# Kernel tuning notes

Measured on AMD Instinct MI355X. Metric: run time of the kernel, lower is better.

Reference implementation:

```python
import jax, jax.numpy as jnp
import numpy as np

HEAD_DIM = 64
N_HEADS = 16
DIM = 1024
EPS = 1e-6
GRID = 32  # make_axial_pos(32, 32)


def _make_theta(head_dim=HEAD_DIM, n_heads=N_HEADS):
    hd8 = head_dim // 8
    nh2 = n_heads // 2
    freqs = np.exp(np.linspace(np.log(np.pi), np.log(10 * np.pi), hd8 * nh2 + 1)[:-1])
    freqs = freqs.reshape(hd8, nh2).T  # (nh2, hd8)
    # axial positions on a 32x32 grid, cell centers in [-1, 1]
    p = np.linspace(-1.0, 1.0, GRID + 1)
    p = (p[:-1] + p[1:]) / 2
    pos = np.stack(np.meshgrid(p, p, indexing='ij'), axis=-1).reshape(GRID * GRID, 2)
    pos = np.concatenate([np.zeros((1, 2)), pos], axis=0)  # (1025, 2)
    th1 = np.concatenate([pos[:-1, None, 0:1] * freqs, pos[:-1, None, 1:2] * freqs], axis=-1)
    th2 = np.concatenate([pos[1:, None, 0:1] * freqs, pos[1:, None, 1:2] * freqs], axis=-1)
    # (seq=1024, n_heads, head_dim//4)
    return np.concatenate([th1, th2], axis=1).astype(np.float32)


def setup_inputs() -> dict:
    key = jax.random.key(0)
    k1, k2, k3 = jax.random.split(key, 3)
    B, S = 8, 1024
    x = jax.random.normal(k1, (B, S, DIM), dtype=jnp.float32)
    scale = jnp.ones((DIM,), dtype=jnp.float32)
    w_qkv = jax.random.normal(k2, (3 * DIM, DIM), dtype=jnp.float32) * 0.02
    w_out = jax.random.normal(k3, (DIM, DIM), dtype=jnp.float32) * 0.02
    theta = jnp.asarray(_make_theta())
    return {"x": x, "scale": scale, "w_qkv": w_qkv, "w_out": w_out, "theta": theta}


def _rms_norm(x, scale, eps):
    xf = x.astype(jnp.float32)
    mean_sq = jnp.mean(xf * xf, axis=-1, keepdims=True)
    s = scale.astype(jnp.float32) * jax.lax.rsqrt(mean_sq + eps)
    return x * s.astype(x.dtype)


def _rope(x, theta):
    # x: (B, H, S, D); theta: (H, S, d) with d = D // 4 -> rotates first D//2 dims
    d = theta.shape[-1]
    cos = jnp.cos(theta)
    sin = jnp.sin(theta)
    x1, x2, rest = x[..., :d], x[..., d:2 * d], x[..., 2 * d:]
    y1 = x1 * cos - x2 * sin
    y2 = x2 * cos + x1 * sin
    return jnp.concatenate([y1, y2, rest], axis=-1)


def reference(x, scale, w_qkv, w_out, theta):
    B, S, dim = x.shape
    H = N_HEADS
    D = dim // H
    skip = x
    xn = _rms_norm(x, scale, EPS)
    qkv = xn @ w_qkv.T                                  # (B, S, 3*dim)
    qkv = qkv.reshape(B, S, 3, H, D).transpose(0, 3, 2, 1, 4)  # (B, H, 3, S, D)
    q, k, v = qkv[:, :, 0], qkv[:, :, 1], qkv[:, :, 2]  # (B, H, S, D)
    th = theta[:S].transpose(1, 0, 2)                   # (H, S, D//4)
    q = _rope(q, th)
    k = _rope(k, th)
    scores = jnp.einsum('bhsd,bhtd->bhst', q, k) / jnp.sqrt(jnp.float32(D))
    causal = jnp.tril(jnp.ones((S, S), dtype=bool))
    scores = jnp.where(causal, scores, jnp.finfo(scores.dtype).min)
    attn = jax.nn.softmax(scores, axis=-1)
    o = jnp.einsum('bhst,bhtd->bhsd', attn, v)          # (B, H, S, D)
    o = o.transpose(0, 2, 1, 3).reshape(B, S, dim)
    return o @ w_out.T + skip
```

## Files before the change

kernel.cpp:

```cpp
#include <hip/hip_runtime.h>
#include <hip/hip_bf16.h>
#include <cstdint>

typedef short short8 __attribute__((ext_vector_type(8)));
typedef float f32x4 __attribute__((ext_vector_type(4)));
typedef unsigned uint4v __attribute__((ext_vector_type(4)));

#define MFMA16(a, b, c) __builtin_amdgcn_mfma_f32_16x16x32_bf16((a), (b), (c), 0, 0, 0)

__device__ __forceinline__ unsigned short f2b(float f) {
    __hip_bfloat16 h = __float2bfloat16(f);
    return __builtin_bit_cast(unsigned short, h);
}

__device__ __forceinline__ void gl_lds16(const void* g, void* l) {
    __builtin_amdgcn_global_load_lds((const __attribute__((address_space(1))) void*)g,
                                     (__attribute__((address_space(3))) void*)l, 16, 0, 0);
}

#define QSC 0.18033688011112042f

__global__ void rmsnorm_kernel(const float* __restrict__ x, const float* __restrict__ scale,
                               unsigned short* __restrict__ xn) {
    const int row = blockIdx.x;
    const int tid = threadIdx.x;
    const float4* xr = (const float4*)(x + (size_t)row * 1024);
    float4 vx = xr[tid];
    float ss = vx.x * vx.x + vx.y * vx.y + vx.z * vx.z + vx.w * vx.w;
#pragma unroll
    for (int m = 1; m < 64; m <<= 1) ss += __shfl_xor(ss, m);
    __shared__ float wsum[4];
    if ((tid & 63) == 0) wsum[tid >> 6] = ss;
    __syncthreads();
    float tot = wsum[0] + wsum[1] + wsum[2] + wsum[3];
    float rs = rsqrtf(tot * (1.0f / 1024.0f) + 1e-6f);
    const float4* sr = (const float4*)scale;
    float4 sv = sr[tid];
    ushort4 r;
    r.x = f2b(vx.x * sv.x * rs);
    r.y = f2b(vx.y * sv.y * rs);
    r.z = f2b(vx.z * sv.z * rs);
    r.w = f2b(vx.w * sv.w * rs);
    *(ushort4*)(xn + (size_t)row * 1024 + tid * 4) = r;
}

__global__ void f2b_kernel(const float* __restrict__ in, unsigned short* __restrict__ outp, int n4) {
    int i = blockIdx.x * 256 + threadIdx.x;
    if (i < n4) {
        float4 vv = ((const float4*)in)[i];
        ushort4 r;
        r.x = f2b(vv.x);
        r.y = f2b(vv.y);
        r.z = f2b(vv.z);
        r.w = f2b(vv.w);
        ((ushort4*)outp)[i] = r;
    }
}

constexpr int BM = 128, BN = 128, BK = 64, KDIM = 1024, NT = KDIM / BK;

template <int EPI>
__launch_bounds__(256, 4) __global__
    void gemm_bt(const unsigned short* __restrict__ A, const unsigned short* __restrict__ Bw,
                 unsigned short* __restrict__ qo, unsigned short* __restrict__ ko,
                 unsigned short* __restrict__ vo, const float* __restrict__ skip,
                 float* __restrict__ out, const float* __restrict__ theta) {
    __shared__ unsigned short As[BM * BK];
    __shared__ unsigned short Bs[BN * BK];
    const int tid = threadIdx.x;
    const int lane = tid & 63, w = tid >> 6;
    const int wr = w >> 1, wc = w & 1;
    const int lr = lane & 15, lg = lane >> 4;
    constexpr int NBX = (EPI == 0) ? 24 : 8;
    const int f = blockIdx.x;
    const int xcd = f & 7, wloc = f >> 3;
    const int g = xcd * (NBX * 8) + wloc;
    const int bx = g % NBX, by = g / NBX;
    const int m0 = by * BM;
    const int n0 = bx * BN;
    const int NCOL = (EPI == 0) ? 3072 : 1024;

    f32x4 acc[4][4] = {};

    auto stage = [&](int kt) {
        const int k0 = kt * BK;
#pragma unroll
        for (int i = 0; i < 4; ++i) {
            int seg = i * 256 + tid;
            int row = seg >> 3, c8 = (seg & 7) ^ (row & 7);
            gl_lds16(A + (size_t)(m0 + row) * KDIM + k0 + c8 * 8, &As[(i * 256 + w * 64) * 8]);
            gl_lds16(Bw + (size_t)(n0 + row) * KDIM + k0 + c8 * 8, &Bs[(i * 256 + w * 64) * 8]);
        }
    };

    for (int kt = 0; kt < NT; ++kt) {
        stage(kt);
        __syncthreads();
#pragma unroll
        for (int kkc = 0; kkc < 2; ++kkc) {
            short8 a[4], b[4];
            const int slot = ((kkc * 4 + lg) ^ (lr & 7)) * 8;
#pragma unroll
            for (int m = 0; m < 4; ++m)
                a[m] = *(const short8*)&As[(wr * 64 + m * 16 + lr) * BK + slot];
#pragma unroll
            for (int n = 0; n < 4; ++n)
                b[n] = *(const short8*)&Bs[(wc * 64 + n * 16 + lr) * BK + slot];
#pragma unroll
            for (int m = 0; m < 4; ++m)
#pragma unroll
                for (int n = 0; n < 4; ++n) acc[m][n] = MFMA16(a[m], b[n], acc[m][n]);
        }
        __syncthreads();
    }

    if (EPI == 0) {
        const int colb = n0 + wc * 64;
        const int c = colb >> 10, h = (colb >> 6) & 15;
#pragma unroll
        for (int m = 0; m < 4; ++m) {
            int grow0 = m0 + wr * 64 + m * 16 + lg * 4;
            int b = grow0 >> 10, s0 = grow0 & 1023;
            if (c == 2) {
#pragma unroll
                for (int n = 0; n < 4; ++n) {
                    int d = n * 16 + lr;
                    ushort4 r;
                    r.x = f2b(acc[m][n][0]);
                    r.y = f2b(acc[m][n][1]);
                    r.z = f2b(acc[m][n][2]);
                    r.w = f2b(acc[m][n][3]);
                    *(ushort4*)&vo[(((size_t)(b * 16 + h)) * 64 + d) * 1024 + s0] = r;
                }
            } else {
                unsigned short* dst = (c == 0) ? qo : ko;
                float sc = (c == 0) ? QSC : 1.0f;
#pragma unroll
                for (int j = 0; j < 4; ++j) {
                    int s = s0 + j;
                    float th = theta[((s * 16 + h) << 4) + lr];
                    float sn, cs;
                    __sincosf(th, &sn, &cs);
                    float x1 = acc[m][0][j], x2 = acc[m][1][j];
                    size_t rowb = (((size_t)(b * 16 + h)) * 1024 + s) * 64;
                    dst[rowb + lr]      = f2b((x1 * cs - x2 * sn) * sc);
                    dst[rowb + 16 + lr] = f2b((x2 * cs + x1 * sn) * sc);
                    dst[rowb + 32 + lr] = f2b(acc[m][2][j] * sc);
                    dst[rowb + 48 + lr] = f2b(acc[m][3][j] * sc);
                }
            }
        }
    } else {
#pragma unroll
        for (int m = 0; m < 4; ++m)
#pragma unroll
            for (int n = 0; n < 4; ++n) {
                int gcol = n0 + wc * 64 + n * 16 + lr;
#pragma unroll
                for (int j = 0; j < 4; ++j) {
                    int grow = m0 + wr * 64 + m * 16 + lg * 4 + j;
                    size_t idx = (size_t)grow * NCOL + gcol;
                    out[idx] = acc[m][n][j] + skip[idx];
                }
            }
    }
}

__launch_bounds__(256, 4) __global__
    void attn_kernel(const unsigned short* __restrict__ q, const unsigned short* __restrict__ k,
                     const unsigned short* __restrict__ vt, unsigned short* __restrict__ o) {
    constexpr int S = 1024, D = 64;
    __shared__ unsigned short Ks[2][64 * 64];
    __shared__ unsigned short Vs[2][64 * 64];
    const int tid = threadIdx.x, lane = tid & 63, w = tid >> 6;
    const int lr = lane & 15, lg = lane >> 4;
    const bool hi4 = (lane & 16) != 0;
    const bool hi5 = (lane & 32) != 0;
    const int f = blockIdx.x;
    const int xcd = f & 7, slot = f >> 3;
    const int bh = xcd * 16 + (slot >> 3);
    const int qmap[8] = {7, 0, 6, 1, 5, 2, 4, 3};
    const int qb = qmap[slot & 7];
    const int qs = qb * 128;
    const size_t base = (size_t)bh * (S * D);
    const int wrow0 = qs + w * 32;

    short8 qf[2][2];
#pragma unroll
    for (int m = 0; m < 2; ++m) {
        const unsigned short* qp = q + base + (size_t)(wrow0 + m * 16 + lr) * D;
        qf[m][0] = *(const short8*)(qp + lg * 8);
        qf[m][1] = *(const short8*)(qp + 32 + lg * 8);
    }

    f32x4 of[2][4] = {};
    float mrun[2] = {-1e30f, -1e30f};
    float lrun[2] = {0.f, 0.f};

    const int nkt = 2 * qb + 2;

    auto stageK = [&](int buf, int kt) {
#pragma unroll
        for (int i = 0; i < 2; ++i) {
            int seg = i * 256 + tid;
            int row = seg >> 3, c8 = (seg & 7) ^ (row & 7);
            gl_lds16(k + base + (size_t)(kt * 64 + row) * D + c8 * 8,
                     &Ks[buf][(i * 256 + w * 64) * 8]);
        }
    };
    auto stageV = [&](int buf, int kt) {
#pragma unroll
        for (int i = 0; i < 2; ++i) {
            int seg = i * 256 + tid;
            int row = seg >> 3, c8 = (seg & 7) ^ (row & 7);
            gl_lds16(vt + base + (size_t)row * S + kt * 64 + c8 * 8,
                     &Vs[buf][(i * 256 + w * 64) * 8]);
        }
    };

    stageK(0, 0);
    stageV(0, 0);
    __syncthreads();

    for (int kt = 0; kt < nkt; ++kt) {
        const int b = kt & 1;
        if (kt + 1 < nkt) {
            stageK(b ^ 1, kt + 1);
            stageV(b ^ 1, kt + 1);
        }

        if (kt * 64 <= wrow0 + 31) {
            f32x4 sf[2][4] = {};
#pragma unroll
            for (int n = 0; n < 4; ++n) {
                const int r = n * 16 + lr;
#pragma unroll
                for (int kkc = 0; kkc < 2; ++kkc) {
                    short8 kf = *(const short8*)&Ks[b][r * 64 + (((kkc * 4 + lg) ^ (lr & 7)) * 8)];
#pragma unroll
                    for (int m = 0; m < 2; ++m) sf[m][n] = MFMA16(kf, qf[m][kkc], sf[m][n]);
                }
            }

            if (kt * 64 + 63 > wrow0) {
#pragma unroll
                for (int m = 0; m < 2; ++m)
#pragma unroll
                    for (int n = 0; n < 4; ++n)
#pragma unroll
                        for (int j = 0; j < 4; ++j) {
                            int t = kt * 64 + 16 * n + lg * 4 + j;
                            int qr = wrow0 + m * 16 + lr;
                            if (t > qr) sf[m][n][j] = -1e30f;
                        }
            }

#pragma unroll
            for (int m = 0; m < 2; ++m) {
                float mx = -1e30f;
#pragma unroll
                for (int n = 0; n < 4; ++n)
                    mx = fmaxf(mx, fmaxf(fmaxf(sf[m][n][0], sf[m][n][1]),
                                         fmaxf(sf[m][n][2], sf[m][n][3])));
                mx = fmaxf(mx, __shfl_xor(mx, 16));
                mx = fmaxf(mx, __shfl_xor(mx, 32));

                if (__any(mx > mrun[m] + 8.0f)) {
                    float newm = fmaxf(mrun[m], mx);
                    float sc = __builtin_amdgcn_exp2f(mrun[m] - newm);
                    mrun[m] = newm;
                    float psum = 0.f;
#pragma unroll
                    for (int n = 0; n < 4; ++n)
#pragma unroll
                        for (int j = 0; j < 4; ++j) {
                            float p = __builtin_amdgcn_exp2f(sf[m][n][j] - newm);
                            sf[m][n][j] = p;
                            psum += p;
                        }
                    lrun[m] = lrun[m] * sc + psum;
#pragma unroll
                    for (int n2 = 0; n2 < 4; ++n2) of[m][n2] *= sc;
                } else {
                    float mo = mrun[m];
                    float psum = 0.f;
#pragma unroll
                    for (int n = 0; n < 4; ++n)
#pragma unroll
                        for (int j = 0; j < 4; ++j) {
                            float p = __builtin_amdgcn_exp2f(sf[m][n][j] - mo);
                            sf[m][n][j] = p;
                            psum += p;
                        }
                    lrun[m] += psum;
                }
            }

            short8 pfrag[2][2];
#pragma unroll
            for (int m = 0; m < 2; ++m) {
                unsigned Dk[4][2];
#pragma unroll
                for (int n = 0; n < 4; ++n)
#pragma unroll
                    for (int w2 = 0; w2 < 2; ++w2)
                        Dk[n][w2] = (unsigned)f2b(sf[m][n][2 * w2]) |
                                    ((unsigned)f2b(sf[m][n][2 * w2 + 1]) << 16);
#pragma unroll
                for (int n1 = 0; n1 < 2; ++n1) {
                    unsigned fr[4];
#pragma unroll
                    for (int w2 = 0; w2 < 2; ++w2) {
                        unsigned A0 = Dk[2 * n1][w2];
                        unsigned A1 = Dk[2 * n1 + 1][w2];
                        unsigned s0 = (unsigned)__shfl_xor((int)A0, 32);
                        unsigned s1 = (unsigned)__shfl_xor((int)A1, 32);
                        unsigned B0 = hi5 ? s1 : A0;
                        unsigned B1 = hi5 ? A1 : s0;
                        s0 = (unsigned)__shfl_xor((int)B0, 16);
                        s1 = (unsigned)__shfl_xor((int)B1, 16);
                        unsigned C0 = hi4 ? s1 : B0;
                        unsigned C1 = hi4 ? B1 : s0;
                        fr[w2] = C0;
                        fr[2 + w2] = C1;
                    }
                    uint4v t4 = {fr[0], fr[1], fr[2], fr[3]};
                    pfrag[m][n1] = __builtin_bit_cast(short8, t4);
                }
            }

#pragma unroll
            for (int kkc = 0; kkc < 2; ++kkc) {
#pragma unroll
                for (int n2 = 0; n2 < 4; ++n2) {
                    const int r = n2 * 16 + lr;
                    short8 av = *(const short8*)&Vs[b][r * 64 + (((kkc * 4 + lg) ^ (lr & 7)) * 8)];
#pragma unroll
                    for (int m = 0; m < 2; ++m) of[m][n2] = MFMA16(av, pfrag[m][kkc], of[m][n2]);
                }
            }
        }

        __syncthreads();
    }

    const int bb = bh >> 4, h = bh & 15;
#pragma unroll
    for (int m = 0; m < 2; ++m) {
        float l = lrun[m];
        l += __shfl_xor(l, 16);
        l += __shfl_xor(l, 32);
        float inv = 1.f / l;
        int srow = wrow0 + m * 16 + lr;
        size_t ob = ((size_t)(bb * 1024 + srow)) * 1024 + h * 64;
#pragma unroll
        for (int n2 = 0; n2 < 4; ++n2) {
            ushort4 r;
            r.x = f2b(of[m][n2][0] * inv);
            r.y = f2b(of[m][n2][1] * inv);
            r.z = f2b(of[m][n2][2] * inv);
            r.w = f2b(of[m][n2][3] * inv);
            *(ushort4*)&o[ob + n2 * 16 + lg * 4] = r;
        }
    }
}

extern "C" void kernel_launch(void* const* d_in, const int* in_sizes, int n_in, void* d_out,
                              int out_size, void* d_ws, size_t ws_size, hipStream_t stream) {
    const float* x = (const float*)d_in[0];
    const float* scale = (const float*)d_in[1];
    const float* w_qkv = (const float*)d_in[2];
    const float* w_out = (const float*)d_in[3];
    const float* theta = (const float*)d_in[4];
    float* out = (float*)d_out;

    char* p = (char*)d_ws;
    unsigned short* xn = (unsigned short*)p;      p += (size_t)8192 * 1024 * 2;
    unsigned short* wqb = (unsigned short*)p;     p += (size_t)3072 * 1024 * 2;
    unsigned short* wob = (unsigned short*)p;     p += (size_t)1024 * 1024 * 2;
    unsigned short* qb_ = (unsigned short*)p;     p += (size_t)128 * 1024 * 64 * 2;
    unsigned short* kb_ = (unsigned short*)p;     p += (size_t)128 * 1024 * 64 * 2;
    unsigned short* vb_ = (unsigned short*)p;     p += (size_t)128 * 1024 * 64 * 2;
    unsigned short* ob_ = (unsigned short*)p;     p += (size_t)8192 * 1024 * 2;

    rmsnorm_kernel<<<8192, 256, 0, stream>>>(x, scale, xn);
    f2b_kernel<<<3072, 256, 0, stream>>>(w_qkv, wqb, 786432);
    f2b_kernel<<<1024, 256, 0, stream>>>(w_out, wob, 262144);
    gemm_bt<0><<<1536, 256, 0, stream>>>(xn, wqb, qb_, kb_, vb_, nullptr, nullptr, theta);
    attn_kernel<<<1024, 256, 0, stream>>>(qb_, kb_, vb_, ob_);
    gemm_bt<1><<<512, 256, 0, stream>>>(ob_, wob, nullptr, nullptr, nullptr, x, out, nullptr);
}
```

Before: 176.0 us.

## Route P through per-wave LDS, swap PV operand order, add MFMA priority hints

Replaces the two-stage cross-lane shuffle transpose of the softmax probabilities with a swizzled write to a small per-wave LDS buffer and a vector read-back, then swaps the A/B operands of the PV MFMA so the output accumulator has a transposed layout. The epilogue is rewritten to match: row sums go through LDS and each lane writes scalar bf16 outputs. The block-to-(head, query-block) mapping is also simplified, and s_setprio is raised around the MFMA sections. This trades shuffle/select ALU work for LDS traffic and extra LDS allocation, and the new scalar output stores are less vectorized than the previous ushort4 stores.

```diff
diff --git a/kernel.cpp b/kernel.cpp
--- a/kernel.cpp
+++ b/kernel.cpp
@@ -4,7 +4,6 @@
 
 typedef short short8 __attribute__((ext_vector_type(8)));
 typedef float f32x4 __attribute__((ext_vector_type(4)));
-typedef unsigned uint4v __attribute__((ext_vector_type(4)));
 
 #define MFMA16(a, b, c) __builtin_amdgcn_mfma_f32_16x16x32_bf16((a), (b), (c), 0, 0, 0)
 
@@ -172,15 +171,13 @@
     constexpr int S = 1024, D = 64;
     __shared__ unsigned short Ks[2][64 * 64];
     __shared__ unsigned short Vs[2][64 * 64];
+    __shared__ unsigned Pls[4][16 * 32];
     const int tid = threadIdx.x, lane = tid & 63, w = tid >> 6;
     const int lr = lane & 15, lg = lane >> 4;
-    const bool hi4 = (lane & 16) != 0;
-    const bool hi5 = (lane & 32) != 0;
     const int f = blockIdx.x;
-    const int xcd = f & 7, slot = f >> 3;
-    const int bh = xcd * 16 + (slot >> 3);
-    const int qmap[8] = {7, 0, 6, 1, 5, 2, 4, 3};
-    const int qb = qmap[slot & 7];
+    const int r0 = f & 127;
+    const int qb = 7 - (f >> 7);
+    const int bh = (r0 & 7) * 16 + (r0 >> 3);
     const int qs = qb * 128;
     const size_t base = (size_t)bh * (S * D);
     const int wrow0 = qs + w * 32;
@@ -218,6 +215,9 @@
         }
     };
 
+    unsigned* Pw = &Pls[w][0];
+    const int swz = (lr & 3) << 3;
+
     stageK(0, 0);
     stageV(0, 0);
     __syncthreads();
@@ -231,6 +231,7 @@
 
         if (kt * 64 <= wrow0 + 31) {
             f32x4 sf[2][4] = {};
+            __builtin_amdgcn_s_setprio(1);
 #pragma unroll
             for (int n = 0; n < 4; ++n) {
                 const int r = n * 16 + lr;
@@ -241,6 +242,7 @@
                     for (int m = 0; m < 2; ++m) sf[m][n] = MFMA16(kf, qf[m][kkc], sf[m][n]);
                 }
             }
+            __builtin_amdgcn_s_setprio(0);
 
             if (kt * 64 + 63 > wrow0) {
 #pragma unroll
@@ -296,7 +298,7 @@
                 }
             }
 
-            short8 pfrag[2][2];
+            short8 pa[2][2];
 #pragma unroll
             for (int m = 0; m < 2; ++m) {
                 unsigned Dk[4][2];
@@ -307,62 +309,52 @@
                         Dk[n][w2] = (unsigned)f2b(sf[m][n][2 * w2]) |
                                     ((unsigned)f2b(sf[m][n][2 * w2 + 1]) << 16);
 #pragma unroll
-                for (int n1 = 0; n1 < 2; ++n1) {
-                    unsigned fr[4];
-#pragma unroll
-                    for (int w2 = 0; w2 < 2; ++w2) {
-                        unsigned A0 = Dk[2 * n1][w2];
-                        unsigned A1 = Dk[2 * n1 + 1][w2];
-                        unsigned s0 = (unsigned)__shfl_xor((int)A0, 32);
-                        unsigned s1 = (unsigned)__shfl_xor((int)A1, 32);
-                        unsigned B0 = hi5 ? s1 : A0;
-                        unsigned B1 = hi5 ? A1 : s0;
-                        s0 = (unsigned)__shfl_xor((int)B0, 16);
-                        s1 = (unsigned)__shfl_xor((int)B1, 16);
-                        unsigned C0 = hi4 ? s1 : B0;
-                        unsigned C1 = hi4 ? B1 : s0;
-                        fr[w2] = C0;
-                        fr[2 + w2] = C1;
-                    }
-                    uint4v t4 = {fr[0], fr[1], fr[2], fr[3]};
-                    pfrag[m][n1] = __builtin_bit_cast(short8, t4);
-                }
-            }
-
+                for (int n = 0; n < 4; ++n)
+#pragma unroll
+                    for (int w2 = 0; w2 < 2; ++w2)
+                        Pw[lr * 32 + ((8 * n + 2 * lg + w2) ^ swz)] = Dk[n][w2];
+#pragma unroll
+                for (int kkc = 0; kkc < 2; ++kkc)
+                    pa[m][kkc] = *(const short8*)&Pw[lr * 32 + ((kkc * 16 + 4 * lg) ^ swz)];
+            }
+
+            __builtin_amdgcn_s_setprio(1);
 #pragma unroll
             for (int kkc = 0; kkc < 2; ++kkc) {
 #pragma unroll
                 for (int n2 = 0; n2 < 4; ++n2) {
                     const int r = n2 * 16 + lr;
-                    short8 av = *(const short8*)&Vs[b][r * 64 + (((kkc * 4 + lg) ^ (lr & 7)) * 8)];
-#pragma unroll
-                    for (int m = 0; m < 2; ++m) of[m][n2] = MFMA16(av, pfrag[m][kkc], of[m][n2]);
-                }
-            }
+                    short8 bv = *(const short8*)&Vs[b][r * 64 + (((kkc * 4 + lg) ^ (lr & 7)) * 8)];
+#pragma unroll
+                    for (int m = 0; m < 2; ++m) of[m][n2] = MFMA16(pa[m][kkc], bv, of[m][n2]);
+                }
+            }
+            __builtin_amdgcn_s_setprio(0);
         }
 
         __syncthreads();
     }
 
-    const int bb = bh >> 4, h = bh & 15;
+    float* Lw = (float*)&Pls[w][0];
 #pragma unroll
     for (int m = 0; m < 2; ++m) {
         float l = lrun[m];
         l += __shfl_xor(l, 16);
         l += __shfl_xor(l, 32);
-        float inv = 1.f / l;
-        int srow = wrow0 + m * 16 + lr;
-        size_t ob = ((size_t)(bb * 1024 + srow)) * 1024 + h * 64;
-#pragma unroll
-        for (int n2 = 0; n2 < 4; ++n2) {
-            ushort4 r;
-            r.x = f2b(of[m][n2][0] * inv);
-            r.y = f2b(of[m][n2][1] * inv);
-            r.z = f2b(of[m][n2][2] * inv);
-            r.w = f2b(of[m][n2][3] * inv);
-            *(ushort4*)&o[ob + n2 * 16 + lg * 4] = r;
-        }
-    }
+        Lw[m * 16 + lr] = l;
+    }
+    const int bb = bh >> 4, h = bh & 15;
+#pragma unroll
+    for (int m = 0; m < 2; ++m)
+#pragma unroll
+        for (int j = 0; j < 4; ++j) {
+            float inv = 1.f / Lw[m * 16 + lg * 4 + j];
+            int srow = wrow0 + m * 16 + lg * 4 + j;
+            size_t ob = ((size_t)(bb * 1024 + srow)) * 1024 + h * 64;
+#pragma unroll
+            for (int n2 = 0; n2 < 4; ++n2)
+                o[ob + n2 * 16 + lr] = f2b(of[m][n2][j] * inv);
+        }
 }
 
 extern "C" void kernel_launch(void* const* d_in, const int* in_sizes, int n_in, void* d_out,
```

New measurement: 161.4 us. 1.09x faster.
